# Optimization experiments

Measured on AMD Instinct MI355X. Metric: run time of the kernel, lower is better.

## Reference

```python
import jax, jax.numpy as jnp
import numpy as np
import math

B, S, D, H = 2, 2048, 512, 8
DK = D // H  # 64
NEG_INF = float('-inf')


def setup_inputs() -> dict:
    key = jax.random.key(0)
    ks = jax.random.split(key, 16)
    s = 1.0 / math.sqrt(D)
    return {
        'in_Q': jax.random.normal(ks[0], (B, S, D), jnp.float32),
        'in_K': jax.random.normal(ks[1], (B, S, D), jnp.float32),
        'in_V': jax.random.normal(ks[2], (B, S, D), jnp.float32),
        'row_pad_mask': jax.random.randint(ks[3], (B, S), 0, 2, jnp.int32),
        'col_pad_mask': jax.random.randint(ks[4], (B, S), 0, 2, jnp.int32),
        'W_Q': jax.random.uniform(ks[5], (D, D), jnp.float32, -s, s),
        'b_Q': jax.random.uniform(ks[6], (D,), jnp.float32, -s, s),
        'W_K': jax.random.uniform(ks[7], (D, D), jnp.float32, -s, s),
        'b_K': jax.random.uniform(ks[8], (D,), jnp.float32, -s, s),
        'W_V': jax.random.uniform(ks[9], (D, D), jnp.float32, -s, s),
        'b_V': jax.random.uniform(ks[10], (D,), jnp.float32, -s, s),
        'W_O': jax.random.uniform(ks[11], (D, D), jnp.float32, -s, s),
        'b_O': jax.random.uniform(ks[12], (D,), jnp.float32, -s, s),
    }


def reference(in_Q, in_K, in_V, row_pad_mask, col_pad_mask,
              W_Q, b_Q, W_K, b_K, W_V, b_V, W_O, b_O):
    b, sq, _ = in_Q.shape
    sk = in_K.shape[1]
    # projections (torch Linear: x @ W.T + b)
    Q = in_Q @ W_Q.T + b_Q
    K = in_K @ W_K.T + b_K
    V = in_V @ W_V.T + b_V
    # chunk along feature dim + stack == reshape to heads: [b, h, s, dk]
    Qh = Q.reshape(b, sq, H, DK).transpose(0, 2, 1, 3)
    Kh = K.reshape(b, sk, H, DK).transpose(0, 2, 1, 3)
    Vh = V.reshape(b, sk, H, DK).transpose(0, 2, 1, 3)
    scores = jnp.einsum('bhqd,bhkd->bhqk', Qh, Kh) / math.sqrt(DK)
    # causal mask (additive -inf above diagonal, as in the original)
    causal = jnp.triu(jnp.full((sq, sk), NEG_INF, scores.dtype), k=1)
    scores = scores + causal
    # padding masks: pad masks encode lengths via their row sums
    row_len = row_pad_mask.sum(axis=1)  # [b]
    col_len = col_pad_mask.sum(axis=1)
    row_np = jnp.arange(sq)[None, :] < row_len[:, None]  # [b, sq]
    col_np = jnp.arange(sk)[None, :] < col_len[:, None]  # [b, sk]
    non_pad = (row_np[:, :, None] & col_np[:, None, :])[:, None]  # [b,1,sq,sk]
    scores = jnp.where(non_pad, scores, NEG_INF)
    p = jax.nn.softmax(scores, axis=-1)
    p = jnp.nan_to_num(p)  # fully-masked rows -> 0 (matches torch nan_to_num)
    attn = jnp.einsum('bhqk,bhkd->bhqd', p, Vh)
    Hcat = attn.transpose(0, 2, 1, 3).reshape(b, sq, D)
    return Hcat @ W_O.T + b_O
```

## Files before the change

kernel.cpp:

```cpp
#include <hip/hip_runtime.h>

#define S_LEN 2048
#define D_MODEL 512
#define NHEAD 8
#define BATCH 2

typedef __attribute__((ext_vector_type(8))) short bf16x8;
typedef __attribute__((ext_vector_type(4))) float f32x4;

__device__ __forceinline__ unsigned short f2bf(float f) {
    union { float f; unsigned u; } v; v.f = f;
    unsigned u = v.u + 0x7FFFu + ((v.u >> 16) & 1u);
    return (unsigned short)(u >> 16);
}

__device__ __forceinline__ void gl_lds16(const unsigned short* g, unsigned short* l) {
    __builtin_amdgcn_global_load_lds(
        (const __attribute__((address_space(1))) void*)g,
        (__attribute__((address_space(3))) void*)l,
        16, 0, 0);
}

__global__ __launch_bounds__(256) void cvtlens_kernel(
    const float* __restrict__ inQ, const float* __restrict__ inK, const float* __restrict__ inV,
    const float* __restrict__ WQ, const float* __restrict__ WK,
    const float* __restrict__ WV, const float* __restrict__ WO,
    const int* __restrict__ rpm, const int* __restrict__ cpm,
    unsigned short* __restrict__ Xbf, unsigned short* __restrict__ Wbf,
    int* __restrict__ lens)
{
    const int t = threadIdx.x;
    if (blockIdx.x < 2) {
        __shared__ int red[256];
        const int b = blockIdx.x;
        int sr = 0, sc2 = 0;
        for (int i = t; i < S_LEN; i += 256) {
            sr  += rpm[b * S_LEN + i];
            sc2 += cpm[b * S_LEN + i];
        }
        red[t] = sr;
        __syncthreads();
        for (int off = 128; off > 0; off >>= 1) {
            if (t < off) red[t] += red[t + off];
            __syncthreads();
        }
        if (t == 0) lens[b * 2 + 0] = red[0];
        __syncthreads();
        red[t] = sc2;
        __syncthreads();
        for (int off = 128; off > 0; off >>= 1) {
            if (t < off) red[t] += red[t + off];
            __syncthreads();
        }
        if (t == 0) lens[b * 2 + 1] = red[0];
    }

    const int NXC = 786432;
    const int NTOT = 917504;
    const int stride = gridDim.x * 256;
    for (int c = blockIdx.x * 256 + t; c < NTOT; c += stride) {
        if (c < NXC) {
            const int flat = c << 3;
            const int z = flat >> 21;
            const int off = flat & 2097151;
            const float* src = ((z == 0) ? inQ : (z == 1) ? inK : inV) + off;
            float4 a = *(const float4*)src;
            float4 d = *(const float4*)(src + 4);
            unsigned short* w = Xbf + flat;
            w[0] = f2bf(a.x); w[1] = f2bf(a.y); w[2] = f2bf(a.z); w[3] = f2bf(a.w);
            w[4] = f2bf(d.x); w[5] = f2bf(d.y); w[6] = f2bf(d.z); w[7] = f2bf(d.w);
        } else {
            const int wflat = (c - NXC) << 3;
            const int wz = wflat >> 18;
            const int off = wflat & 262143;
            const float* src = ((wz == 0) ? WQ : (wz == 1) ? WK : (wz == 2) ? WV : WO) + off;
            float4 a = *(const float4*)src;
            float4 d = *(const float4*)(src + 4);
            unsigned short* w = Wbf + wflat;
            w[0] = f2bf(a.x); w[1] = f2bf(a.y); w[2] = f2bf(a.z); w[3] = f2bf(a.w);
            w[4] = f2bf(d.x); w[5] = f2bf(d.y); w[6] = f2bf(d.z); w[7] = f2bf(d.w);
        }
    }
}

__global__ __launch_bounds__(256) void proj_gemm(
    const unsigned short* __restrict__ Xbf, const unsigned short* __restrict__ Wbf,
    const float* __restrict__ bQ, const float* __restrict__ bK, const float* __restrict__ bV,
    const int* __restrict__ lens,
    unsigned short* __restrict__ Qg, unsigned short* __restrict__ Kg,
    unsigned short* __restrict__ VTg)
{
    __shared__ __align__(16) unsigned short Xld[128 * 64];
    __shared__ __align__(16) unsigned short Wld[128 * 64];

    const int z = blockIdx.z;
    const int tileS = blockIdx.x * 128;
    const int tileF = blockIdx.y * 128;
    const int bb0 = tileS >> 11;
    const int rl = lens[bb0 * 2], cl = lens[bb0 * 2 + 1];
    const int limit = (z == 0) ? rl : cl;
    if ((tileS & 2047) >= limit) return;

    const unsigned short* X = Xbf + (size_t)z * (4096 * 512);
    const unsigned short* W = Wbf + (size_t)z * (512 * 512);
    const float* bias = (z == 0) ? bQ : (z == 1) ? bK : bV;

    const int t = threadIdx.x;
    const int wv = t >> 6, lane = t & 63, l15 = lane & 15, quad = lane >> 4;
    const int ro = lane >> 3;
    const int lc8 = ((lane & 7) ^ ro) * 8;

    const unsigned short* gX = X + (size_t)(tileS + wv * 32 + ro) * 512 + lc8;
    const unsigned short* gW = W + (size_t)(tileF + wv * 32 + ro) * 512 + lc8;
    unsigned short* lX0 = Xld + wv * 2048;
    unsigned short* lW0 = Wld + wv * 2048;

    const int f_off = (wv & 1) * 64, s_off = (wv >> 1) * 64;
    const int swk = l15 & 7;

    f32x4 acc[4][4] = {};

    for (int kk = 0; kk < 8; ++kk) {
        if (kk) __syncthreads();
        const int k0 = kk * 64;
        #pragma unroll
        for (int j = 0; j < 4; ++j) {
            gl_lds16(gX + j * 8 * 512 + k0, lX0 + j * 512);
            gl_lds16(gW + j * 8 * 512 + k0, lW0 + j * 512);
        }
        __syncthreads();
        #pragma unroll
        for (int kk2 = 0; kk2 < 2; ++kk2) {
            bf16x8 wf[4], xf[4];
            #pragma unroll
            for (int i = 0; i < 4; ++i) {
                const int rw = f_off + i * 16 + l15;
                wf[i] = *(const bf16x8*)(Wld + rw * 64 + ((kk2 * 4 + quad) ^ swk) * 8);
                const int rx = s_off + i * 16 + l15;
                xf[i] = *(const bf16x8*)(Xld + rx * 64 + ((kk2 * 4 + quad) ^ swk) * 8);
            }
            #pragma unroll
            for (int ft = 0; ft < 4; ++ft)
                #pragma unroll
                for (int st = 0; st < 4; ++st)
                    acc[ft][st] = __builtin_amdgcn_mfma_f32_16x16x32_bf16(
                        wf[ft], xf[st], acc[ft][st], 0, 0, 0);
        }
    }

    const float oscale = (z == 0) ? 0.125f : 1.0f;
    #pragma unroll
    for (int ft = 0; ft < 4; ++ft) {
        const int f = tileF + f_off + ft * 16 + quad * 4;
        const int h = f >> 6, dk = f & 63;
        const float b0 = bias[f], b1 = bias[f + 1], b2 = bias[f + 2], b3 = bias[f + 3];
        #pragma unroll
        for (int st = 0; st < 4; ++st) {
            const int s = tileS + s_off + st * 16 + l15;
            const int bb = s >> 11, seq = s & 2047;
            const f32x4 a = acc[ft][st];
            if (z <= 1) {
                unsigned short* dst = ((z == 0) ? Qg : Kg)
                    + ((size_t)((bb * 8 + h) * 2048 + seq)) * 64 + dk;
                ushort4 u;
                u.x = f2bf((a[0] + b0) * oscale); u.y = f2bf((a[1] + b1) * oscale);
                u.z = f2bf((a[2] + b2) * oscale); u.w = f2bf((a[3] + b3) * oscale);
                *(ushort4*)dst = u;
            } else {
                unsigned short* dst = VTg
                    + ((size_t)((bb * 8 + h) * 64 + dk)) * 2048 + seq;
                dst[0]    = f2bf(a[0] + b0);
                dst[2048] = f2bf(a[1] + b1);
                dst[4096] = f2bf(a[2] + b2);
                dst[6144] = f2bf(a[3] + b3);
            }
        }
    }
}

__global__ __launch_bounds__(256) void attn_kernel(
    const unsigned short* __restrict__ Qg, const unsigned short* __restrict__ Kg,
    const unsigned short* __restrict__ VTg, const int* __restrict__ lens,
    unsigned short* __restrict__ AO)
{
    __shared__ __align__(16) unsigned short Pl[4 * 16 * 72];
    __shared__ __align__(16) float Po[4 * 16 * 68];
    __shared__ float Ml[4 * 16];
    __shared__ float Ll[4 * 16];

    const int t = threadIdx.x;
    const int wv = t >> 6, lane = t & 63, l15 = lane & 15, quad = lane >> 4;
    const int bh = blockIdx.y;
    const int b = bh >> 3, h = bh & 7;
    const int q0 = blockIdx.x * 16;
    const int rl = lens[b * 2], cl = lens[b * 2 + 1];

    if (q0 >= rl) {
        const int row = t >> 4, cg = t & 15;
        ushort4 zz = {0, 0, 0, 0};
        *(ushort4*)(AO + ((size_t)(b * 2048 + q0 + row)) * 512 + h * 64 + cg * 4) = zz;
        return;
    }

    const unsigned short* Qrow = Qg + ((size_t)(bh * 2048 + q0 + l15)) * 64;
    const bf16x8 aq0 = *(const bf16x8*)(Qrow + quad * 8);
    const bf16x8 aq1 = *(const bf16x8*)(Qrow + 32 + quad * 8);

    unsigned short* pb = Pl + wv * (16 * 72);

    f32x4 oacc[4] = {};
    float m_[4], l_[4];
    #pragma unroll
    for (int r = 0; r < 4; ++r) { m_[r] = -__builtin_inff(); l_[r] = 0.f; }

    const int q_end = q0 + 16;
    const int kv_max = (cl < q_end) ? cl : q_end;
    const int ntiles = (kv_max + 63) >> 6;
    const int qrow0 = q0 + quad * 4;

    for (int kt = wv; kt < ntiles; kt += 4) {
        const int kv0 = kt * 64;
        f32x4 sc[4] = {};
        #pragma unroll
        for (int ct = 0; ct < 4; ++ct) {
            const unsigned short* Krow = Kg + ((size_t)(bh * 2048 + kv0 + ct * 16 + l15)) * 64;
            sc[ct] = __builtin_amdgcn_mfma_f32_16x16x32_bf16(
                aq0, *(const bf16x8*)(Krow + quad * 8), sc[ct], 0, 0, 0);
            sc[ct] = __builtin_amdgcn_mfma_f32_16x16x32_bf16(
                aq1, *(const bf16x8*)(Krow + 32 + quad * 8), sc[ct], 0, 0, 0);
        }

        const bool full = (kv0 + 64 <= q0) && (kv0 + 64 <= cl) && (q_end <= rl);

        #pragma unroll
        for (int r = 0; r < 4; ++r) {
            const int q = qrow0 + r;
            float mx = -__builtin_inff();
            if (full) {
                #pragma unroll
                for (int ct = 0; ct < 4; ++ct) mx = fmaxf(mx, sc[ct][r]);
            } else {
                #pragma unroll
                for (int ct = 0; ct < 4; ++ct) {
                    const int kv = kv0 + ct * 16 + l15;
                    float s = sc[ct][r];
                    const bool valid = (q < rl) && (kv < cl) && (kv <= q);
                    s = valid ? s : -__builtin_inff();
                    sc[ct][r] = s;
                    mx = fmaxf(mx, s);
                }
            }
            mx = fmaxf(mx, __shfl_xor(mx, 1, 16));
            mx = fmaxf(mx, __shfl_xor(mx, 2, 16));
            mx = fmaxf(mx, __shfl_xor(mx, 4, 16));
            mx = fmaxf(mx, __shfl_xor(mx, 8, 16));

            const float mold = m_[r];
            const float mnew = fmaxf(mold, mx);
            const float alpha = (mold == -__builtin_inff()) ? 0.f : __expf(mold - mnew);
            float psum = 0.f;
            #pragma unroll
            for (int ct = 0; ct < 4; ct++) {
                const float sv = sc[ct][r];
                const float p = (mnew == -__builtin_inff()) ? 0.f : __expf(sv - mnew);
                sc[ct][r] = p;
                psum += p;
            }
            psum += __shfl_xor(psum, 1, 16);
            psum += __shfl_xor(psum, 2, 16);
            psum += __shfl_xor(psum, 4, 16);
            psum += __shfl_xor(psum, 8, 16);
            l_[r] = alpha * l_[r] + psum;
            m_[r] = mnew;
            #pragma unroll
            for (int ct = 0; ct < 4; ct++) oacc[ct][r] *= alpha;
        }

        #pragma unroll
        for (int ct = 0; ct < 4; ++ct) {
            #pragma unroll
            for (int r = 0; r < 4; ++r)
                pb[(quad * 4 + r) * 72 + ct * 16 + l15] = f2bf(sc[ct][r]);
        }
        const bf16x8 pf0 = *(const bf16x8*)(pb + l15 * 72 + quad * 8);
        const bf16x8 pf1 = *(const bf16x8*)(pb + l15 * 72 + 32 + quad * 8);
        #pragma unroll
        for (int ct = 0; ct < 4; ++ct) {
            const unsigned short* Vrow = VTg + ((size_t)(bh * 64 + ct * 16 + l15)) * 2048 + kv0;
            oacc[ct] = __builtin_amdgcn_mfma_f32_16x16x32_bf16(
                pf0, *(const bf16x8*)(Vrow + quad * 8), oacc[ct], 0, 0, 0);
            oacc[ct] = __builtin_amdgcn_mfma_f32_16x16x32_bf16(
                pf1, *(const bf16x8*)(Vrow + 32 + quad * 8), oacc[ct], 0, 0, 0);
        }
    }

    #pragma unroll
    for (int ct = 0; ct < 4; ++ct) {
        #pragma unroll
        for (int r = 0; r < 4; ++r)
            Po[wv * 1088 + (quad * 4 + r) * 68 + ct * 16 + l15] = oacc[ct][r];
    }
    if (l15 == 0) {
        #pragma unroll
        for (int r = 0; r < 4; ++r) {
            Ml[wv * 16 + quad * 4 + r] = m_[r];
            Ll[wv * 16 + quad * 4 + r] = l_[r];
        }
    }
    __syncthreads();

    const int row = t >> 4, cg = t & 15;
    float mw[4];
    float mstar = -__builtin_inff();
    #pragma unroll
    for (int w = 0; w < 4; ++w) {
        mw[w] = Ml[w * 16 + row];
        mstar = fmaxf(mstar, mw[w]);
    }
    f32x4 o = {};
    if (mstar != -__builtin_inff()) {
        float lst = 0.f;
        #pragma unroll
        for (int w = 0; w < 4; ++w) {
            const float sw = (mw[w] == -__builtin_inff()) ? 0.f : __expf(mw[w] - mstar);
            lst += sw * Ll[w * 16 + row];
            const f32x4 pv = *(const f32x4*)&Po[w * 1088 + row * 68 + cg * 4];
            o[0] += sw * pv[0]; o[1] += sw * pv[1];
            o[2] += sw * pv[2]; o[3] += sw * pv[3];
        }
        const float inv = (lst > 0.f) ? 1.f / lst : 0.f;
        o[0] *= inv; o[1] *= inv; o[2] *= inv; o[3] *= inv;
    }
    ushort4 u;
    u.x = f2bf(o[0]); u.y = f2bf(o[1]); u.z = f2bf(o[2]); u.w = f2bf(o[3]);
    *(ushort4*)(AO + ((size_t)(b * 2048 + q0 + row)) * 512 + h * 64 + cg * 4) = u;
}

__global__ __launch_bounds__(256) void out_gemm(
    const unsigned short* __restrict__ AO, const unsigned short* __restrict__ Wbf,
    const float* __restrict__ bO, const int* __restrict__ lens, float* __restrict__ out)
{
    __shared__ __align__(16) unsigned short Xld[128 * 64];
    __shared__ __align__(16) unsigned short Wld[128 * 64];

    const int tileS = blockIdx.x * 128;
    const int tileF = blockIdx.y * 128;
    const int bb0 = tileS >> 11;
    const int rl = lens[bb0 * 2];
    const int t = threadIdx.x;

    if ((tileS & 2047) >= rl) {
        const int r0 = t >> 2;
        const int cg = (t & 3) * 32;
        float4 bv[8];
        #pragma unroll
        for (int j = 0; j < 8; ++j) bv[j] = *(const float4*)(bO + tileF + cg + j * 4);
        #pragma unroll
        for (int i = 0; i < 2; ++i) {
            float* orow = out + (size_t)(tileS + i * 64 + r0) * 512 + tileF + cg;
            #pragma unroll
            for (int j = 0; j < 8; ++j) *(float4*)(orow + j * 4) = bv[j];
        }
        return;
    }

    const unsigned short* W = Wbf + (size_t)3 * (512 * 512);
    const int wv = t >> 6, lane = t & 63, l15 = lane & 15, quad = lane >> 4;
    const int ro = lane >> 3;
    const int lc8 = ((lane & 7) ^ ro) * 8;

    const unsigned short* gX = AO + (size_t)(tileS + wv * 32 + ro) * 512 + lc8;
    const unsigned short* gW = W + (size_t)(tileF + wv * 32 + ro) * 512 + lc8;
    unsigned short* lX0 = Xld + wv * 2048;
    unsigned short* lW0 = Wld + wv * 2048;

    const int f_off = (wv & 1) * 64, s_off = (wv >> 1) * 64;
    const int swk = l15 & 7;

    f32x4 acc[4][4] = {};

    for (int kk = 0; kk < 8; ++kk) {
        if (kk) __syncthreads();
        const int k0 = kk * 64;
        #pragma unroll
        for (int j = 0; j < 4; ++j) {
            gl_lds16(gX + j * 8 * 512 + k0, lX0 + j * 512);
            gl_lds16(gW + j * 8 * 512 + k0, lW0 + j * 512);
        }
        __syncthreads();
        #pragma unroll
        for (int kk2 = 0; kk2 < 2; ++kk2) {
            bf16x8 wf[4], xf[4];
            #pragma unroll
            for (int i = 0; i < 4; ++i) {
                const int rw = f_off + i * 16 + l15;
                wf[i] = *(const bf16x8*)(Wld + rw * 64 + ((kk2 * 4 + quad) ^ swk) * 8);
                const int rx = s_off + i * 16 + l15;
                xf[i] = *(const bf16x8*)(Xld + rx * 64 + ((kk2 * 4 + quad) ^ swk) * 8);
            }
            #pragma unroll
            for (int ft = 0; ft < 4; ++ft)
                #pragma unroll
                for (int st = 0; st < 4; ++st)
                    acc[ft][st] = __builtin_amdgcn_mfma_f32_16x16x32_bf16(
                        wf[ft], xf[st], acc[ft][st], 0, 0, 0);
        }
    }

    #pragma unroll
    for (int ft = 0; ft < 4; ++ft) {
        const int f = tileF + f_off + ft * 16 + quad * 4;
        const float4 bv = *(const float4*)(bO + f);
        #pragma unroll
        for (int st = 0; st < 4; ++st) {
            const int s = tileS + s_off + st * 16 + l15;
            float4 o;
            o.x = acc[ft][st][0] + bv.x;
            o.y = acc[ft][st][1] + bv.y;
            o.z = acc[ft][st][2] + bv.z;
            o.w = acc[ft][st][3] + bv.w;
            *(float4*)(out + (size_t)s * 512 + f) = o;
        }
    }
}

extern "C" void kernel_launch(void* const* d_in, const int* in_sizes, int n_in,
                              void* d_out, int out_size, void* d_ws, size_t ws_size,
                              hipStream_t stream)
{
    const float* inQ = (const float*)d_in[0];
    const float* inK = (const float*)d_in[1];
    const float* inV = (const float*)d_in[2];
    const int*   rpm = (const int*)d_in[3];
    const int*   cpm = (const int*)d_in[4];
    const float* WQ  = (const float*)d_in[5];
    const float* bQ  = (const float*)d_in[6];
    const float* WK  = (const float*)d_in[7];
    const float* bK  = (const float*)d_in[8];
    const float* WV  = (const float*)d_in[9];
    const float* bV  = (const float*)d_in[10];
    const float* WO  = (const float*)d_in[11];
    const float* bO  = (const float*)d_in[12];
    float* out = (float*)d_out;

    char* ws = (char*)d_ws;
    unsigned short* Xbf = (unsigned short*)(ws);
    unsigned short* Wbf = (unsigned short*)(ws + 12582912);
    unsigned short* Qg  = (unsigned short*)(ws + 14680064);
    unsigned short* Kg  = (unsigned short*)(ws + 18874368);
    unsigned short* VTg = (unsigned short*)(ws + 23068672);
    unsigned short* AO  = (unsigned short*)(ws + 27262976);
    int* lens           = (int*)(ws + 31457280);

    cvtlens_kernel<<<dim3(1792), dim3(256), 0, stream>>>(
        inQ, inK, inV, WQ, WK, WV, WO, rpm, cpm, Xbf, Wbf, lens);
    proj_gemm<<<dim3(32, 4, 3), dim3(256), 0, stream>>>(
        Xbf, Wbf, bQ, bK, bV, lens, Qg, Kg, VTg);
    attn_kernel<<<dim3(128, 16), dim3(256), 0, stream>>>(Qg, Kg, VTg, lens, AO);
    out_gemm<<<dim3(32, 4), dim3(256), 0, stream>>>(AO, Wbf, bO, lens, out);
}
```

Baseline: 158.0 us.

## Double-buffer GEMM LDS tiles and stage attention K/V through swizzled LDS

After: 151.7 us, median of 2. -4.0%, faster.

```diff
diff --git a/kernel.cpp b/kernel.cpp
--- a/kernel.cpp
+++ b/kernel.cpp
@@ -90,8 +90,8 @@
     unsigned short* __restrict__ Qg, unsigned short* __restrict__ Kg,
     unsigned short* __restrict__ VTg)
 {
-    __shared__ __align__(16) unsigned short Xld[128 * 64];
-    __shared__ __align__(16) unsigned short Wld[128 * 64];
+    __shared__ __align__(16) unsigned short Xld[2][8192];
+    __shared__ __align__(16) unsigned short Wld[2][8192];
 
     const int z = blockIdx.z;
     const int tileS = blockIdx.x * 128;
@@ -112,32 +112,41 @@
 
     const unsigned short* gX = X + (size_t)(tileS + wv * 32 + ro) * 512 + lc8;
     const unsigned short* gW = W + (size_t)(tileF + wv * 32 + ro) * 512 + lc8;
-    unsigned short* lX0 = Xld + wv * 2048;
-    unsigned short* lW0 = Wld + wv * 2048;
+    const int wvo = wv * 2048;
 
     const int f_off = (wv & 1) * 64, s_off = (wv >> 1) * 64;
     const int swk = l15 & 7;
 
     f32x4 acc[4][4] = {};
 
+    #pragma unroll
+    for (int j = 0; j < 4; ++j) {
+        gl_lds16(gX + j * 4096, &Xld[0][wvo + j * 512]);
+        gl_lds16(gW + j * 4096, &Wld[0][wvo + j * 512]);
+    }
+
     for (int kk = 0; kk < 8; ++kk) {
-        if (kk) __syncthreads();
-        const int k0 = kk * 64;
-        #pragma unroll
-        for (int j = 0; j < 4; ++j) {
-            gl_lds16(gX + j * 8 * 512 + k0, lX0 + j * 512);
-            gl_lds16(gW + j * 8 * 512 + k0, lW0 + j * 512);
-        }
         __syncthreads();
+        if (kk < 7) {
+            const int k0 = (kk + 1) * 64;
+            const int nb = (kk + 1) & 1;
+            #pragma unroll
+            for (int j = 0; j < 4; ++j) {
+                gl_lds16(gX + k0 + j * 4096, &Xld[nb][wvo + j * 512]);
+                gl_lds16(gW + k0 + j * 4096, &Wld[nb][wvo + j * 512]);
+            }
+        }
+        const unsigned short* Xb = Xld[kk & 1];
+        const unsigned short* Wb = Wld[kk & 1];
         #pragma unroll
         for (int kk2 = 0; kk2 < 2; ++kk2) {
             bf16x8 wf[4], xf[4];
             #pragma unroll
             for (int i = 0; i < 4; ++i) {
                 const int rw = f_off + i * 16 + l15;
-                wf[i] = *(const bf16x8*)(Wld + rw * 64 + ((kk2 * 4 + quad) ^ swk) * 8);
+                wf[i] = *(const bf16x8*)(Wb + rw * 64 + ((kk2 * 4 + quad) ^ swk) * 8);
                 const int rx = s_off + i * 16 + l15;
-                xf[i] = *(const bf16x8*)(Xld + rx * 64 + ((kk2 * 4 + quad) ^ swk) * 8);
+                xf[i] = *(const bf16x8*)(Xb + rx * 64 + ((kk2 * 4 + quad) ^ swk) * 8);
             }
             #pragma unroll
             for (int ft = 0; ft < 4; ++ft)
@@ -183,10 +192,11 @@
     const unsigned short* __restrict__ VTg, const int* __restrict__ lens,
     unsigned short* __restrict__ AO)
 {
-    __shared__ __align__(16) unsigned short Pl[4 * 16 * 72];
-    __shared__ __align__(16) float Po[4 * 16 * 68];
-    __shared__ float Ml[4 * 16];
-    __shared__ float Ll[4 * 16];
+    __shared__ __align__(16) char smem[32768 + 9216 + 512];
+    unsigned short* stage = (unsigned short*)smem;
+    unsigned short* Plb   = (unsigned short*)(smem + 32768);
+    float* Ml = (float*)(smem + 32768 + 9216);
+    float* Ll = Ml + 64;
 
     const int t = threadIdx.x;
     const int wv = t >> 6, lane = t & 63, l15 = lane & 15, quad = lane >> 4;
@@ -206,7 +216,14 @@
     const bf16x8 aq0 = *(const bf16x8*)(Qrow + quad * 8);
     const bf16x8 aq1 = *(const bf16x8*)(Qrow + 32 + quad * 8);
 
-    unsigned short* pb = Pl + wv * (16 * 72);
+    unsigned short* stw = stage + wv * 4096;
+    unsigned short* pb  = Plb + wv * (16 * 72);
+
+    const int sro = lane >> 3;
+    const int sc8 = ((lane & 7) ^ sro) * 8;
+    const int kg_off  = sro * 64 + sc8;
+    const int vtg_off = sro * 2048 + sc8;
+    const int sw7 = l15 & 7;
 
     f32x4 oacc[4] = {};
     float m_[4], l_[4];
@@ -220,14 +237,31 @@
 
     for (int kt = wv; kt < ntiles; kt += 4) {
         const int kv0 = kt * 64;
+
+        {
+            const unsigned short* kg = Kg + ((size_t)(bh * 2048 + kv0)) * 64 + kg_off;
+            #pragma unroll
+            for (int j = 0; j < 8; ++j)
+                gl_lds16(kg + j * 512, stw + j * 512);
+        }
+        __builtin_amdgcn_s_waitcnt(0x0070);
+
         f32x4 sc[4] = {};
         #pragma unroll
         for (int ct = 0; ct < 4; ++ct) {
-            const unsigned short* Krow = Kg + ((size_t)(bh * 2048 + kv0 + ct * 16 + l15)) * 64;
-            sc[ct] = __builtin_amdgcn_mfma_f32_16x16x32_bf16(
-                aq0, *(const bf16x8*)(Krow + quad * 8), sc[ct], 0, 0, 0);
-            sc[ct] = __builtin_amdgcn_mfma_f32_16x16x32_bf16(
-                aq1, *(const bf16x8*)(Krow + 32 + quad * 8), sc[ct], 0, 0, 0);
+            const unsigned short* krow = stw + (ct * 16 + l15) * 64;
+            const bf16x8 kf0 = *(const bf16x8*)(krow + ((quad    ) ^ sw7) * 8);
+            const bf16x8 kf1 = *(const bf16x8*)(krow + ((quad + 4) ^ sw7) * 8);
+            sc[ct] = __builtin_amdgcn_mfma_f32_16x16x32_bf16(aq0, kf0, sc[ct], 0, 0, 0);
+            sc[ct] = __builtin_amdgcn_mfma_f32_16x16x32_bf16(aq1, kf1, sc[ct], 0, 0, 0);
+        }
+        __builtin_amdgcn_s_waitcnt(0x0070);
+
+        {
+            const unsigned short* vg = VTg + ((size_t)(bh * 64)) * 2048 + kv0 + vtg_off;
+            #pragma unroll
+            for (int j = 0; j < 8; ++j)
+                gl_lds16(vg + j * 16384, stw + j * 512);
         }
 
         const bool full = (kv0 + 64 <= q0) && (kv0 + 64 <= cl) && (q_end <= rl);
@@ -284,28 +318,33 @@
         }
         const bf16x8 pf0 = *(const bf16x8*)(pb + l15 * 72 + quad * 8);
         const bf16x8 pf1 = *(const bf16x8*)(pb + l15 * 72 + 32 + quad * 8);
+
+        __builtin_amdgcn_s_waitcnt(0x0070);
         #pragma unroll
         for (int ct = 0; ct < 4; ++ct) {
-            const unsigned short* Vrow = VTg + ((size_t)(bh * 64 + ct * 16 + l15)) * 2048 + kv0;
-            oacc[ct] = __builtin_amdgcn_mfma_f32_16x16x32_bf16(
-                pf0, *(const bf16x8*)(Vrow + quad * 8), oacc[ct], 0, 0, 0);
-            oacc[ct] = __builtin_amdgcn_mfma_f32_16x16x32_bf16(
-                pf1, *(const bf16x8*)(Vrow + 32 + quad * 8), oacc[ct], 0, 0, 0);
-        }
-    }
-
-    #pragma unroll
-    for (int ct = 0; ct < 4; ++ct) {
-        #pragma unroll
-        for (int r = 0; r < 4; ++r)
-            Po[wv * 1088 + (quad * 4 + r) * 68 + ct * 16 + l15] = oacc[ct][r];
-    }
+            const unsigned short* vrow = stw + (ct * 16 + l15) * 64;
+            const bf16x8 vf0 = *(const bf16x8*)(vrow + ((quad    ) ^ sw7) * 8);
+            const bf16x8 vf1 = *(const bf16x8*)(vrow + ((quad + 4) ^ sw7) * 8);
+            oacc[ct] = __builtin_amdgcn_mfma_f32_16x16x32_bf16(pf0, vf0, oacc[ct], 0, 0, 0);
+            oacc[ct] = __builtin_amdgcn_mfma_f32_16x16x32_bf16(pf1, vf1, oacc[ct], 0, 0, 0);
+        }
+    }
+
     if (l15 == 0) {
         #pragma unroll
         for (int r = 0; r < 4; ++r) {
             Ml[wv * 16 + quad * 4 + r] = m_[r];
             Ll[wv * 16 + quad * 4 + r] = l_[r];
         }
+    }
+    __syncthreads();
+
+    float* Po = (float*)smem;
+    #pragma unroll
+    for (int ct = 0; ct < 4; ++ct) {
+        #pragma unroll
+        for (int r = 0; r < 4; ++r)
+            Po[wv * 1088 + (quad * 4 + r) * 68 + ct * 16 + l15] = oacc[ct][r];
     }
     __syncthreads();
 
@@ -340,8 +379,8 @@
     const unsigned short* __restrict__ AO, const unsigned short* __restrict__ Wbf,
     const float* __restrict__ bO, const int* __restrict__ lens, float* __restrict__ out)
 {
-    __shared__ __align__(16) unsigned short Xld[128 * 64];
-    __shared__ __align__(16) unsigned short Wld[128 * 64];
+    __shared__ __align__(16) unsigned short Xld[2][8192];
+    __shared__ __align__(16) unsigned short Wld[2][8192];
 
     const int tileS = blockIdx.x * 128;
     const int tileF = blockIdx.y * 128;
@@ -371,32 +410,41 @@
 
     const unsigned short* gX = AO + (size_t)(tileS + wv * 32 + ro) * 512 + lc8;
     const unsigned short* gW = W + (size_t)(tileF + wv * 32 + ro) * 512 + lc8;
-    unsigned short* lX0 = Xld + wv * 2048;
-    unsigned short* lW0 = Wld + wv * 2048;
+    const int wvo = wv * 2048;
 
     const int f_off = (wv & 1) * 64, s_off = (wv >> 1) * 64;
     const int swk = l15 & 7;
 
     f32x4 acc[4][4] = {};
 
+    #pragma unroll
+    for (int j = 0; j < 4; ++j) {
+        gl_lds16(gX + j * 4096, &Xld[0][wvo + j * 512]);
+        gl_lds16(gW + j * 4096, &Wld[0][wvo + j * 512]);
+    }
+
     for (int kk = 0; kk < 8; ++kk) {
-        if (kk) __syncthreads();
-        const int k0 = kk * 64;
-        #pragma unroll
-        for (int j = 0; j < 4; ++j) {
-            gl_lds16(gX + j * 8 * 512 + k0, lX0 + j * 512);
-            gl_lds16(gW + j * 8 * 512 + k0, lW0 + j * 512);
-        }
         __syncthreads();
+        if (kk < 7) {
+            const int k0 = (kk + 1) * 64;
+            const int nb = (kk + 1) & 1;
+            #pragma unroll
+            for (int j = 0; j < 4; ++j) {
+                gl_lds16(gX + k0 + j * 4096, &Xld[nb][wvo + j * 512]);
+                gl_lds16(gW + k0 + j * 4096, &Wld[nb][wvo + j * 512]);
+            }
+        }
+        const unsigned short* Xb = Xld[kk & 1];
+        const unsigned short* Wb = Wld[kk & 1];
         #pragma unroll
         for (int kk2 = 0; kk2 < 2; ++kk2) {
             bf16x8 wf[4], xf[4];
             #pragma unroll
             for (int i = 0; i < 4; ++i) {
                 const int rw = f_off + i * 16 + l15;
-                wf[i] = *(const bf16x8*)(Wld + rw * 64 + ((kk2 * 4 + quad) ^ swk) * 8);
+                wf[i] = *(const bf16x8*)(Wb + rw * 64 + ((kk2 * 4 + quad) ^ swk) * 8);
                 const int rx = s_off + i * 16 + l15;
-                xf[i] = *(const bf16x8*)(Xld + rx * 64 + ((kk2 * 4 + quad) ^ swk) * 8);
+                xf[i] = *(const bf16x8*)(Xb + rx * 64 + ((kk2 * 4 + quad) ^ swk) * 8);
             }
             #pragma unroll
             for (int ft = 0; ft < 4; ++ft)
```
